# Performance work log

Measured on AMD Instinct MI355X. Metric: run time of the kernel, lower is better.

## Reference

```python
import jax, jax.numpy as jnp
import numpy as np

GROUP_SIZES = (64, 128, 256, 96, 160, 224, 192, 288, 320, 112, 80, 48, 32, 16, 32)
LENGTH = 512
ALPHABET = 21


def setup_inputs() -> dict:
    key = jax.random.key(0)
    keys = jax.random.split(key, len(GROUP_SIZES) + 1)
    n_samples = int(sum(GROUP_SIZES))
    inp = {"x": jax.random.normal(keys[0], (n_samples, LENGTH, ALPHABET), dtype=jnp.float32)}
    for i, g in enumerate(GROUP_SIZES):
        inp[f"mat{i}"] = jax.random.normal(keys[i + 1], (g, g), dtype=jnp.float32)
    return inp


def reference(x, mat0, mat1, mat2, mat3, mat4, mat5, mat6, mat7, mat8, mat9,
              mat10, mat11, mat12, mat13, mat14):
    mats = (mat0, mat1, mat2, mat3, mat4, mat5, mat6, mat7, mat8, mat9,
            mat10, mat11, mat12, mat13, mat14)
    # Block-diagonal grouped matmul along the sample dim: out[sl] = mats_i @ x[sl].
    # Group boundaries are static Python ints, so slicing is jit-friendly.
    pieces = []
    start = 0
    for m, g in zip(mats, GROUP_SIZES):
        xg = x[start:start + g]  # (g, L, A)
        pieces.append(jnp.einsum('gh,hla->gla', m, xg))
        start += g
    return jnp.concatenate(pieces, axis=0)
```

## Files before the change

kernel.cpp:

```cpp
#include <hip/hip_runtime.h>

#define NCOL 10752
#define NG 15
#define NTILES 23
#define WS_NEED 1064960

typedef __bf16 bf16;
typedef __attribute__((ext_vector_type(8))) __bf16 bf16x8;
typedef __attribute__((ext_vector_type(4))) __bf16 bf16x4;
typedef __attribute__((ext_vector_type(4))) float f32x4;

__constant__ int c_gsize[NG]  = {64,128,256,96,160,224,192,288,320,112,80,48,32,16,32};
__constant__ int c_gstart[NG] = {0,64,192,448,544,704,928,1120,1408,1728,1840,1920,1968,2000,2016};
__constant__ int c_tgrp[NTILES]  = {8,8,8,7,7,7,2,2,5,5,6,6,4,4,1,9,3,10,0,11,12,14,13};
__constant__ int c_trow[NTILES]  = {0,128,256,0,128,256,0,128,0,128,0,128,0,128,0,0,0,0,0,0,0,0,0};
__constant__ int c_niter[NTILES] = {10,10,10,9,9,9,8,8,7,7,6,6,5,5,4,4,3,3,2,2,1,1,1};
__constant__ int c_tbase[NTILES] = {0,10,20,30,39,48,57,65,73,80,87,93,99,104,109,113,117,120,123,125,127,128,129};

struct MatPtrs { const float* p[NG]; };

constexpr int BM = 128, BN = 128, BK = 32, BKp = 40;

__global__ __launch_bounds__(256)
void prep_kernel(MatPtrs mats, bf16* __restrict__ ws)
{
    const int kt = blockIdx.x, tile = blockIdx.y;
    if (kt >= c_niter[tile]) return;
    const int grp  = c_tgrp[tile];
    const int row0 = c_trow[tile];
    const int g    = c_gsize[grp];
    const float* __restrict__ M = mats.p[grp];
    bf16* dst = ws + (size_t)(c_tbase[tile] + kt) * 4096;

    #pragma unroll
    for (int h = 0; h < 2; h++) {
        const int u    = threadIdx.x + h * 256;
        const int l    = u & 63;
        const int st   = u >> 6;
        const int row  = row0 + st * 16 + (l & 15);
        const int kcol = kt * 32 + (l >> 4) * 8;
        bf16x8 w = {};
        if (row < g && kcol < g) {
            const float* src = M + (size_t)row * g + kcol;
            #pragma unroll
            for (int j = 0; j < 8; j++) w[j] = (bf16)src[j];
        }
        *(bf16x8*)(dst + (size_t)u * 8) = w;
    }
}

__global__ __launch_bounds__(256, 4)
void matapply_kernel(const float* __restrict__ x, const bf16* __restrict__ aws,
                     float* __restrict__ out)
{
    __shared__ bf16 sA[2][4096];
    __shared__ bf16 sB[2][BN][BKp];

    const int tid    = threadIdx.x;
    const int colb   = blockIdx.x * BN;
    const int tileid = blockIdx.y;

    const int grp  = c_tgrp[tileid];
    const int g    = c_gsize[grp];
    const int s    = c_gstart[grp];
    const int row0 = c_trow[tileid];
    const bf16* __restrict__ aimg = aws + (size_t)c_tbase[tileid] * 4096;

    const int wave = tid >> 6;
    const int lane = tid & 63;
    const int wr   = (wave & 1) * 64;
    const int wc   = (wave >> 1) * 64;
    const int lm   = lane & 15;
    const int kq   = lane >> 4;
    const int kb   = kq * 8;

    const int bC = (tid & 31) * 4;
    const int bK = (tid >> 5) * 4;

    const int nIter = (g + BK - 1) / BK;

    f32x4 acc[4][4];
    #pragma unroll
    for (int i = 0; i < 4; i++)
        #pragma unroll
        for (int j = 0; j < 4; j++)
            acc[i][j] = (f32x4){0.f, 0.f, 0.f, 0.f};

    float4 xv[4];

    auto glds_a = [&](int buf, int kt) {
        const bf16* src = aimg + (size_t)kt * 4096 + (size_t)(wave * 2) * 512 + lane * 8;
        #pragma unroll
        for (int c = 0; c < 2; c++)
            __builtin_amdgcn_global_load_lds(
                (const __attribute__((address_space(1))) unsigned int*)(src + c * 512),
                (__attribute__((address_space(3))) unsigned int*)&sA[buf][(wave * 2 + c) * 512],
                16, 0, 0);
    };

    glds_a(0, 0);
    #pragma unroll
    for (int j = 0; j < 4; j++)
        xv[j] = *(const float4*)(x + (size_t)(s + bK + j) * NCOL + colb + bC);
    #pragma unroll
    for (int cc = 0; cc < 4; cc++) {
        int lc = bC + cc;
        bf16x4 w;
        #pragma unroll
        for (int j = 0; j < 4; j++)
            w[j] = (bf16)(((const float*)&xv[j])[cc]);
        *(bf16x4*)&sB[0][lc][bK ^ (((lc >> 2) & 3) << 3)] = w;
    }
    __syncthreads();

    for (int it = 0; it < nIter; ++it) {
        const int cur = it & 1;
        const bool more = (it + 1) < nIter;

        if (more) {
            glds_a(1 - cur, it + 1);
            const int k0 = (it + 1) * BK;
            #pragma unroll
            for (int j = 0; j < 4; j++)
                xv[j] = *(const float4*)(x + (size_t)(s + k0 + bK + j) * NCOL + colb + bC);
        }

        bf16x8 af[4], bfr[4];
        #pragma unroll
        for (int i = 0; i < 4; i++)
            af[i] = *(const bf16x8*)&sA[cur][((wave & 1) * 4 + i) * 512 + lane * 8];
        #pragma unroll
        for (int j = 0; j < 4; j++) {
            int lc = wc + j * 16 + lm;
            bfr[j] = *(const bf16x8*)&sB[cur][lc][kb ^ (((lc >> 2) & 3) << 3)];
        }
        #pragma unroll
        for (int i = 0; i < 4; i++)
            #pragma unroll
            for (int j = 0; j < 4; j++)
                acc[i][j] = __builtin_amdgcn_mfma_f32_16x16x32_bf16(af[i], bfr[j], acc[i][j], 0, 0, 0);

        if (more) {
            const int nxt = 1 - cur;
            #pragma unroll
            for (int cc = 0; cc < 4; cc++) {
                int lc = bC + cc;
                bf16x4 w;
                #pragma unroll
                for (int j = 0; j < 4; j++)
                    w[j] = (bf16)(((const float*)&xv[j])[cc]);
                *(bf16x4*)&sB[nxt][lc][bK ^ (((lc >> 2) & 3) << 3)] = w;
            }
            __syncthreads();
        }
    }

    #pragma unroll
    for (int i = 0; i < 4; i++) {
        #pragma unroll
        for (int r = 0; r < 4; r++) {
            int row = row0 + wr + i * 16 + kq * 4 + r;
            if (row < g) {
                float* orow = out + (size_t)(s + row) * NCOL + colb + wc;
                #pragma unroll
                for (int j = 0; j < 4; j++)
                    orow[j * 16 + lm] = acc[i][j][r];
            }
        }
    }
}

__global__ __launch_bounds__(256)
void matapply_fb(const float* __restrict__ x, MatPtrs mats, float* __restrict__ out)
{
    __shared__ bf16 sA[2][BM][BKp];
    __shared__ bf16 sB[2][BN][BKp];

    const int tid    = threadIdx.x;
    const int colb   = blockIdx.x * BN;
    const int tileid = blockIdx.y;

    const int grp  = c_tgrp[tileid];
    const int row0 = c_trow[tileid];
    const int g    = c_gsize[grp];
    const int s    = c_gstart[grp];
    const float* __restrict__ M = mats.p[grp];

    const int wave = tid >> 6;
    const int lane = tid & 63;
    const int wr   = (wave & 1) * 64;
    const int wc   = (wave >> 1) * 64;
    const int lm   = lane & 15;
    const int kq   = lane >> 4;
    const int kb   = kq * 8;

    const int aK = (tid & 7) * 4;
    const int aR = tid >> 3;
    const int bC = (tid & 31) * 4;
    const int bK = (tid >> 5) * 4;

    const int nIter = (g + BK - 1) / BK;

    f32x4 acc[4][4];
    #pragma unroll
    for (int i = 0; i < 4; i++)
        #pragma unroll
        for (int j = 0; j < 4; j++)
            acc[i][j] = (f32x4){0.f, 0.f, 0.f, 0.f};

    float4 av[4], xv[4];

    #pragma unroll
    for (int i = 0; i < 4; i++) {
        int r = aR + 32 * i;
        av[i] = make_float4(0.f, 0.f, 0.f, 0.f);
        if ((row0 + r) < g && aK < g)
            av[i] = *(const float4*)(M + (size_t)(row0 + r) * g + aK);
    }
    #pragma unroll
    for (int j = 0; j < 4; j++)
        xv[j] = *(const float4*)(x + (size_t)(s + bK + j) * NCOL + colb + bC);

    #pragma unroll
    for (int i = 0; i < 4; i++) {
        int r = aR + 32 * i;
        bf16x4 w;
        w[0] = (bf16)av[i].x; w[1] = (bf16)av[i].y; w[2] = (bf16)av[i].z; w[3] = (bf16)av[i].w;
        *(bf16x4*)&sA[0][r][aK] = w;
    }
    #pragma unroll
    for (int cc = 0; cc < 4; cc++) {
        int lc = bC + cc;
        bf16x4 w;
        #pragma unroll
        for (int j = 0; j < 4; j++)
            w[j] = (bf16)(((const float*)&xv[j])[cc]);
        *(bf16x4*)&sB[0][lc][bK ^ (((lc >> 2) & 3) << 3)] = w;
    }
    __syncthreads();

    for (int it = 0; it < nIter; ++it) {
        const int cur = it & 1;
        const bool more = (it + 1) < nIter;

        if (more) {
            const int k0 = (it + 1) * BK;
            #pragma unroll
            for (int i = 0; i < 4; i++) {
                int r = aR + 32 * i;
                av[i] = make_float4(0.f, 0.f, 0.f, 0.f);
                if ((row0 + r) < g && (k0 + aK) < g)
                    av[i] = *(const float4*)(M + (size_t)(row0 + r) * g + k0 + aK);
            }
            #pragma unroll
            for (int j = 0; j < 4; j++)
                xv[j] = *(const float4*)(x + (size_t)(s + k0 + bK + j) * NCOL + colb + bC);
        }

        bf16x8 af[4], bfr[4];
        #pragma unroll
        for (int i = 0; i < 4; i++)
            af[i] = *(const bf16x8*)&sA[cur][wr + i * 16 + lm][kb];
        #pragma unroll
        for (int j = 0; j < 4; j++) {
            int lc = wc + j * 16 + lm;
            bfr[j] = *(const bf16x8*)&sB[cur][lc][kb ^ (((lc >> 2) & 3) << 3)];
        }
        #pragma unroll
        for (int i = 0; i < 4; i++)
            #pragma unroll
            for (int j = 0; j < 4; j++)
                acc[i][j] = __builtin_amdgcn_mfma_f32_16x16x32_bf16(af[i], bfr[j], acc[i][j], 0, 0, 0);

        if (more) {
            const int nxt = 1 - cur;
            #pragma unroll
            for (int i = 0; i < 4; i++) {
                int r = aR + 32 * i;
                bf16x4 w;
                w[0] = (bf16)av[i].x; w[1] = (bf16)av[i].y; w[2] = (bf16)av[i].z; w[3] = (bf16)av[i].w;
                *(bf16x4*)&sA[nxt][r][aK] = w;
            }
            #pragma unroll
            for (int cc = 0; cc < 4; cc++) {
                int lc = bC + cc;
                bf16x4 w;
                #pragma unroll
                for (int j = 0; j < 4; j++)
                    w[j] = (bf16)(((const float*)&xv[j])[cc]);
                *(bf16x4*)&sB[nxt][lc][bK ^ (((lc >> 2) & 3) << 3)] = w;
            }
            __syncthreads();
        }
    }

    #pragma unroll
    for (int i = 0; i < 4; i++) {
        #pragma unroll
        for (int r = 0; r < 4; r++) {
            int row = row0 + wr + i * 16 + kq * 4 + r;
            if (row < g) {
                float* orow = out + (size_t)(s + row) * NCOL + colb + wc;
                #pragma unroll
                for (int j = 0; j < 4; j++)
                    orow[j * 16 + lm] = acc[i][j][r];
            }
        }
    }
}

extern "C" void kernel_launch(void* const* d_in, const int* in_sizes, int n_in,
                              void* d_out, int out_size, void* d_ws, size_t ws_size,
                              hipStream_t stream)
{
    const float* x = (const float*)d_in[0];
    MatPtrs mp;
    for (int i = 0; i < NG; i++) mp.p[i] = (const float*)d_in[1 + i];
    float* out = (float*)d_out;

    if (d_ws != nullptr && ws_size >= (size_t)WS_NEED) {
        prep_kernel<<<dim3(10, NTILES), dim3(256), 0, stream>>>(mp, (bf16*)d_ws);
        matapply_kernel<<<dim3(NCOL / BN, NTILES), dim3(256), 0, stream>>>(
            x, (const bf16*)d_ws, out);
    } else {
        matapply_fb<<<dim3(NCOL / BN, NTILES), dim3(256), 0, stream>>>(x, mp, out);
    }
}
```

Baseline: 192.8 us.

## Deepen matapply pipeline to prefetch two K-steps ahead with manual waitcnt barriers

Converts the main grouped-matmul kernel from a double-buffered to a deeper pipeline. A tiles move to a triple-buffered LDS ring loaded two iterations ahead via global_load_lds. x loads are issued two steps ahead and converted into the B buffer one step ahead. __syncthreads is replaced by explicit s_waitcnt vmcnt/lgkmcnt plus s_barrier with sched_barriers, so in-flight global loads can overlap the MFMAs. The occupancy hint of 4 is dropped from launch bounds, which together with the extra LDS buffer and registers may lower waves per CU. The hand-tuned vmcnt counts are also fragile if the compiler reorders loads.

```diff
diff --git a/kernel.cpp b/kernel.cpp
--- a/kernel.cpp
+++ b/kernel.cpp
@@ -49,11 +49,11 @@
     }
 }
 
-__global__ __launch_bounds__(256, 4)
+__global__ __launch_bounds__(256)
 void matapply_kernel(const float* __restrict__ x, const bf16* __restrict__ aws,
                      float* __restrict__ out)
 {
-    __shared__ bf16 sA[2][4096];
+    __shared__ bf16 sA[3][4096];
     __shared__ bf16 sB[2][BN][BKp];
 
     const int tid    = threadIdx.x;
@@ -98,37 +98,55 @@
                 16, 0, 0);
     };
 
+    auto stageB = [&](int buf, const float4* v) {
+        #pragma unroll
+        for (int cc = 0; cc < 4; cc++) {
+            int lc = bC + cc;
+            bf16x4 w;
+            #pragma unroll
+            for (int j = 0; j < 4; j++)
+                w[j] = (bf16)(((const float*)&v[j])[cc]);
+            *(bf16x4*)&sB[buf][lc][bK ^ (((lc >> 2) & 3) << 3)] = w;
+        }
+    };
+
     glds_a(0, 0);
+    if (nIter > 1) glds_a(1, 1);
+    float4 xp[4];
     #pragma unroll
     for (int j = 0; j < 4; j++)
-        xv[j] = *(const float4*)(x + (size_t)(s + bK + j) * NCOL + colb + bC);
-    #pragma unroll
-    for (int cc = 0; cc < 4; cc++) {
-        int lc = bC + cc;
-        bf16x4 w;
+        xp[j] = *(const float4*)(x + (size_t)(s + bK + j) * NCOL + colb + bC);
+    if (nIter > 1) {
         #pragma unroll
         for (int j = 0; j < 4; j++)
-            w[j] = (bf16)(((const float*)&xv[j])[cc]);
-        *(bf16x4*)&sB[0][lc][bK ^ (((lc >> 2) & 3) << 3)] = w;
-    }
-    __syncthreads();
+            xv[j] = *(const float4*)(x + (size_t)(s + BK + bK + j) * NCOL + colb + bC);
+    }
+    stageB(0, xp);
+    asm volatile("s_waitcnt vmcnt(4) lgkmcnt(0)" ::: "memory");
+    __builtin_amdgcn_sched_barrier(0);
+    __builtin_amdgcn_s_barrier();
+    __builtin_amdgcn_sched_barrier(0);
 
     for (int it = 0; it < nIter; ++it) {
-        const int cur = it & 1;
-        const bool more = (it + 1) < nIter;
-
-        if (more) {
-            glds_a(1 - cur, it + 1);
-            const int k0 = (it + 1) * BK;
+        const int  cur = it & 1;
+        const bool w1  = (it + 1) < nIter;
+        const bool w2  = (it + 2) < nIter;
+
+        if (w1) stageB(1 - cur, xv);
+
+        if (w2) {
+            glds_a((it + 2) % 3, it + 2);
+            const int k0 = (it + 2) * BK;
             #pragma unroll
             for (int j = 0; j < 4; j++)
                 xv[j] = *(const float4*)(x + (size_t)(s + k0 + bK + j) * NCOL + colb + bC);
         }
 
         bf16x8 af[4], bfr[4];
+        const int ab = it % 3;
         #pragma unroll
         for (int i = 0; i < 4; i++)
-            af[i] = *(const bf16x8*)&sA[cur][((wave & 1) * 4 + i) * 512 + lane * 8];
+            af[i] = *(const bf16x8*)&sA[ab][((wave & 1) * 4 + i) * 512 + lane * 8];
         #pragma unroll
         for (int j = 0; j < 4; j++) {
             int lc = wc + j * 16 + lm;
@@ -140,18 +158,12 @@
             for (int j = 0; j < 4; j++)
                 acc[i][j] = __builtin_amdgcn_mfma_f32_16x16x32_bf16(af[i], bfr[j], acc[i][j], 0, 0, 0);
 
-        if (more) {
-            const int nxt = 1 - cur;
-            #pragma unroll
-            for (int cc = 0; cc < 4; cc++) {
-                int lc = bC + cc;
-                bf16x4 w;
-                #pragma unroll
-                for (int j = 0; j < 4; j++)
-                    w[j] = (bf16)(((const float*)&xv[j])[cc]);
-                *(bf16x4*)&sB[nxt][lc][bK ^ (((lc >> 2) & 3) << 3)] = w;
-            }
-            __syncthreads();
+        if (w1) {
+            if (w2) { asm volatile("s_waitcnt vmcnt(6) lgkmcnt(0)" ::: "memory"); }
+            else    { asm volatile("s_waitcnt vmcnt(0) lgkmcnt(0)" ::: "memory"); }
+            __builtin_amdgcn_sched_barrier(0);
+            __builtin_amdgcn_s_barrier();
+            __builtin_amdgcn_sched_barrier(0);
         }
     }
 
@@ -173,8 +185,8 @@
 __global__ __launch_bounds__(256)
 void matapply_fb(const float* __restrict__ x, MatPtrs mats, float* __restrict__ out)
 {
-    __shared__ bf16 sA[2][BM][BKp];
-    __shared__ bf16 sB[2][BN][BKp];
+    __shared__ bf16 sAf[2][BM][BKp];
+    __shared__ bf16 sBf[2][BN][BKp];
 
     const int tid    = threadIdx.x;
     const int colb   = blockIdx.x * BN;
@@ -226,7 +238,7 @@
         int r = aR + 32 * i;
         bf16x4 w;
         w[0] = (bf16)av[i].x; w[1] = (bf16)av[i].y; w[2] = (bf16)av[i].z; w[3] = (bf16)av[i].w;
-        *(bf16x4*)&sA[0][r][aK] = w;
+        *(bf16x4*)&sAf[0][r][aK] = w;
     }
     #pragma unroll
     for (int cc = 0; cc < 4; cc++) {
@@ -235,7 +247,7 @@
         #pragma unroll
         for (int j = 0; j < 4; j++)
             w[j] = (bf16)(((const float*)&xv[j])[cc]);
-        *(bf16x4*)&sB[0][lc][bK ^ (((lc >> 2) & 3) << 3)] = w;
+        *(bf16x4*)&sBf[0][lc][bK ^ (((lc >> 2) & 3) << 3)] = w;
     }
     __syncthreads();
 
@@ -260,11 +272,11 @@
         bf16x8 af[4], bfr[4];
         #pragma unroll
         for (int i = 0; i < 4; i++)
-            af[i] = *(const bf16x8*)&sA[cur][wr + i * 16 + lm][kb];
+            af[i] = *(const bf16x8*)&sAf[cur][wr + i * 16 + lm][kb];
         #pragma unroll
         for (int j = 0; j < 4; j++) {
             int lc = wc + j * 16 + lm;
-            bfr[j] = *(const bf16x8*)&sB[cur][lc][kb ^ (((lc >> 2) & 3) << 3)];
+            bfr[j] = *(const bf16x8*)&sBf[cur][lc][kb ^ (((lc >> 2) & 3) << 3)];
         }
         #pragma unroll
         for (int i = 0; i < 4; i++)
@@ -279,7 +291,7 @@
                 int r = aR + 32 * i;
                 bf16x4 w;
                 w[0] = (bf16)av[i].x; w[1] = (bf16)av[i].y; w[2] = (bf16)av[i].z; w[3] = (bf16)av[i].w;
-                *(bf16x4*)&sA[nxt][r][aK] = w;
+                *(bf16x4*)&sAf[nxt][r][aK] = w;
             }
             #pragma unroll
             for (int cc = 0; cc < 4; cc++) {
@@ -288,7 +300,7 @@
                 #pragma unroll
                 for (int j = 0; j < 4; j++)
                     w[j] = (bf16)(((const float*)&xv[j])[cc]);
-                *(bf16x4*)&sB[nxt][lc][bK ^ (((lc >> 2) & 3) << 3)] = w;
+                *(bf16x4*)&sBf[nxt][lc][bK ^ (((lc >> 2) & 3) << 3)] = w;
             }
             __syncthreads();
         }
```

Result: no change. 193.5 us (+0.4%).
